# Kernel tuning notes

Measured on AMD Instinct MI355X. Metric: run time of the kernel, lower is better.

The kernel has to match this reference:

```python
import jax, jax.numpy as jnp
import numpy as np

N0 = 16384; F_IN = 384; H = 512; E0 = 131072
DEPTH = 2; RATIO = 0.25; START_K = 6; K_INC = 1; INTERP_K = 6


def _pdist2(a, b):
    # squared euclidean distances [Na, Nb]
    d2 = jnp.sum(a * a, axis=1)[:, None] + jnp.sum(b * b, axis=1)[None, :] - 2.0 * (a @ b.T)
    return jnp.maximum(d2, 0.0)


def _fps(pos, n_keep):
    # farthest point sampling, deterministic start at node 0
    sel0 = jnp.zeros((n_keep,), jnp.int32)
    dist0 = jnp.sum((pos - pos[0]) ** 2, axis=-1)

    def body(i, st):
        sel, dist = st
        idx = jnp.argmax(dist).astype(jnp.int32)
        sel = sel.at[i].set(idx)
        dist = jnp.minimum(dist, jnp.sum((pos - pos[idx]) ** 2, axis=-1))
        return (sel, dist)

    sel, _ = jax.lax.fori_loop(1, n_keep, body, (sel0, dist0))
    return sel


def _knn_graph(pos, k):
    n = pos.shape[0]
    d2 = _pdist2(pos, pos)
    d2 = d2.at[jnp.arange(n), jnp.arange(n)].set(1e10)  # exclude self
    _, nbr = jax.lax.top_k(-d2, k)                      # [n, k] nearest neighbors
    src = nbr.reshape(-1)                               # flow: source_to_target
    dst = jnp.repeat(jnp.arange(n, dtype=nbr.dtype), k)
    return src, dst


def _gcn(x, src, dst, W, b):
    # GCNConv(improved=True): A_hat = D^-1/2 (A + 2I) D^-1/2, edge weights = 1
    n = x.shape[0]
    h = x @ W
    deg = jax.ops.segment_sum(jnp.ones(src.shape[0], x.dtype), dst, num_segments=n) + 2.0
    dinv = jax.lax.rsqrt(deg)
    coef = dinv[src] * dinv[dst]
    agg = jax.ops.segment_sum(h[src] * coef[:, None], dst, num_segments=n)
    agg = agg + h * (2.0 * dinv * dinv)[:, None]        # self loops with weight 2
    return agg + b


def _knn_interpolate(x, pos_x, pos_y, k):
    # interpolate coarse features x at pos_x onto fine positions pos_y (PyG knn_interpolate)
    d2 = _pdist2(pos_y, pos_x)                          # [Ny, Nx]
    negd, idx = jax.lax.top_k(-d2, k)                   # k nearest coarse points
    w = 1.0 / jnp.maximum(-negd, 1e-16)                 # [Ny, k]
    num = jnp.einsum('yk,ykf->yf', w, x[idx])
    return num / jnp.sum(w, axis=-1, keepdims=True)


def setup_inputs() -> dict:
    key = jax.random.key(0)
    ks = jax.random.split(key, 16)
    def w(k, fin, fout):
        return (jax.random.normal(k, (fin, fout), jnp.float32) / np.sqrt(fin)).astype(jnp.float32)
    return {
        'x': jax.random.normal(ks[0], (N0, F_IN), jnp.float32),
        'pos': jax.random.uniform(ks[1], (N0, 2), jnp.float32) * 100.0,
        'edge_index': jax.random.randint(ks[2], (2, E0), 0, N0, dtype=jnp.int32),
        'W_down0': w(ks[3], F_IN, H), 'b_down0': jnp.zeros((H,), jnp.float32),
        'W_down1': w(ks[4], H, H),   'b_down1': jnp.zeros((H,), jnp.float32),
        'W_up0': w(ks[5], H, H),     'b_up0': jnp.zeros((H,), jnp.float32),
        'W_up1': w(ks[6], H, H),     'b_up1': jnp.zeros((H,), jnp.float32),
        'W_lin': w(ks[7], H, H),     'b_lin': jnp.zeros((H,), jnp.float32),
    }


def reference(x, pos, edge_index, W_down0, b_down0, W_down1, b_down1,
              W_up0, b_up0, W_up1, b_up1, W_lin, b_lin):
    src, dst = edge_index[0], edge_index[1]
    Wd = [(W_down0, b_down0), (W_down1, b_down1)]
    Wu = [(W_up0, b_up0), (W_up1, b_up1)]
    all_pos = [pos]
    all_edges = [(src, dst)]
    for i in range(DEPTH):
        x = jax.nn.relu(_gcn(x, src, dst, *Wd[i]))
        n_keep = int(x.shape[0] * RATIO)
        perm = _fps(jax.lax.stop_gradient(pos), n_keep)
        pos = pos[perm]
        src, dst = _knn_graph(pos, START_K + i * K_INC)
        x = x[perm]
        all_pos.append(pos)
        all_edges.append((src, dst))
    for i in range(DEPTH):
        x = _knn_interpolate(x, all_pos[-i - 1], all_pos[-i - 2], INTERP_K)
        s, d = all_edges[-i - 2]
        x = jax.nn.relu(_gcn(x, s, d, *Wu[i]))
    return x @ W_lin + b_lin
```

## Files before the change

### kernel.cpp

```cpp
#include <hip/hip_runtime.h>

#define N0 16384
#define N1 4096
#define N2 1024
#define E0C 131072
#define FIN 384
#define HF 512

__device__ inline float4 f4fma(float w, const float4 v, float4 a) {
  a.x = fmaf(w, v.x, a.x); a.y = fmaf(w, v.y, a.y);
  a.z = fmaf(w, v.z, a.z); a.w = fmaf(w, v.w, a.w);
  return a;
}

__global__ __launch_bounds__(256)
void count_deg(const int* __restrict__ dst, int* __restrict__ cnt, int E) {
  int e = blockIdx.x * 256 + threadIdx.x;
  if (e < E) atomicAdd(&cnt[dst[e]], 1);
}

__global__ __launch_bounds__(1024)
void scan_offsets(const int* __restrict__ cnt, int* __restrict__ offs,
                  float* __restrict__ dinv) {
  __shared__ int ts[1024];
  const int t = threadIdx.x;
  int local[16];
  int sum = 0;
  #pragma unroll
  for (int j = 0; j < 16; ++j) { local[j] = cnt[t * 16 + j]; sum += local[j]; }
  ts[t] = sum;
  __syncthreads();
  for (int off = 1; off < 1024; off <<= 1) {
    int v = (t >= off) ? ts[t - off] : 0;
    __syncthreads();
    ts[t] += v;
    __syncthreads();
  }
  int run = ts[t] - sum;
  #pragma unroll
  for (int j = 0; j < 16; ++j) {
    offs[t * 16 + j] = run;
    dinv[t * 16 + j] = 1.0f / sqrtf((float)local[j] + 2.0f);
    run += local[j];
  }
  if (t == 1023) offs[N0] = run;
}

__global__ __launch_bounds__(256)
void fill_csr(const int* __restrict__ src, const int* __restrict__ dst,
              const int* __restrict__ offs, int* __restrict__ cursor,
              int* __restrict__ srcl, int E) {
  int e = blockIdx.x * 256 + threadIdx.x;
  if (e < E) {
    int d = dst[e];
    int p = atomicAdd(&cursor[d], 1);
    srcl[offs[d] + p] = src[e];
  }
}

template<int BM, int BN, int BK>
__global__ __launch_bounds__(256)
void gemm_f32(const float* __restrict__ A, const float* __restrict__ W,
              const float* __restrict__ bias, float* __restrict__ C,
              int M, int N, int K, int addBias) {
  __shared__ float As[BK][BM + 4];
  __shared__ float Ws[BK][BN];
  const int tid = threadIdx.x;
  const int bm = blockIdx.x * BM;
  const int bn = blockIdx.y * BN;
  const int tx = tid & 15;
  const int ty = tid >> 4;
  float acc[8][4];
  #pragma unroll
  for (int i = 0; i < 8; ++i)
    #pragma unroll
    for (int j = 0; j < 4; ++j) acc[i][j] = 0.f;

  for (int k0 = 0; k0 < K; k0 += BK) {
    #pragma unroll
    for (int h = 0; h < (BM * BK) / (256 * 4); ++h) {
      int q = tid + h * 256;
      int r = q >> 2;
      int c = (q & 3) << 2;
      float4 v = *(const float4*)(A + (size_t)(bm + r) * K + k0 + c);
      As[c][r] = v.x; As[c + 1][r] = v.y; As[c + 2][r] = v.z; As[c + 3][r] = v.w;
    }
    {
      int kk = tid >> 4;
      int n = (tid & 15) << 2;
      *(float4*)(&Ws[kk][n]) = *(const float4*)(W + (size_t)(k0 + kk) * N + bn + n);
    }
    __syncthreads();
    #pragma unroll
    for (int kk = 0; kk < BK; ++kk) {
      float4 b4 = *(const float4*)(&Ws[kk][tx << 2]);
      float4 a0 = *(const float4*)(&As[kk][ty << 3]);
      float4 a1 = *(const float4*)(&As[kk][(ty << 3) + 4]);
      float a[8] = {a0.x, a0.y, a0.z, a0.w, a1.x, a1.y, a1.z, a1.w};
      float b[4] = {b4.x, b4.y, b4.z, b4.w};
      #pragma unroll
      for (int i = 0; i < 8; ++i)
        #pragma unroll
        for (int j = 0; j < 4; ++j)
          acc[i][j] = fmaf(a[i], b[j], acc[i][j]);
    }
    __syncthreads();
  }
  #pragma unroll
  for (int i = 0; i < 8; ++i) {
    int row = bm + (ty << 3) + i;
    float4 o = {acc[i][0], acc[i][1], acc[i][2], acc[i][3]};
    if (addBias) {
      const float4 bb = *(const float4*)(bias + bn + (tx << 2));
      o.x += bb.x; o.y += bb.y; o.z += bb.z; o.w += bb.w;
    }
    *(float4*)(C + (size_t)row * N + bn + (tx << 2)) = o;
  }
}

__global__ __launch_bounds__(256)
void gcn_agg_csr(const float* __restrict__ h, const int* __restrict__ offs,
                 const int* __restrict__ srcl, const float* __restrict__ dinv,
                 const float* __restrict__ bias, float* __restrict__ out, int n) {
  const int wid = threadIdx.x >> 6, lane = threadIdx.x & 63;
  const int node = blockIdx.x * 4 + wid;
  if (node >= n) return;
  const float di = dinv[node];
  const int s0 = offs[node], s1 = offs[node + 1];
  float4 a0 = {0, 0, 0, 0}, a1 = {0, 0, 0, 0};
  for (int e = s0; e < s1; ++e) {
    const int s = srcl[e];
    const float w = dinv[s] * di;
    const float4* r = (const float4*)(h + (size_t)s * HF);
    a0 = f4fma(w, r[lane], a0);
    a1 = f4fma(w, r[64 + lane], a1);
  }
  const float sw = 2.0f * di * di;
  const float4* rs = (const float4*)(h + (size_t)node * HF);
  a0 = f4fma(sw, rs[lane], a0);
  a1 = f4fma(sw, rs[64 + lane], a1);
  const float4 b0 = *(const float4*)(bias + (lane << 2));
  const float4 b1 = *(const float4*)(bias + 256 + (lane << 2));
  a0.x = fmaxf(a0.x + b0.x, 0.f); a0.y = fmaxf(a0.y + b0.y, 0.f);
  a0.z = fmaxf(a0.z + b0.z, 0.f); a0.w = fmaxf(a0.w + b0.w, 0.f);
  a1.x = fmaxf(a1.x + b1.x, 0.f); a1.y = fmaxf(a1.y + b1.y, 0.f);
  a1.z = fmaxf(a1.z + b1.z, 0.f); a1.w = fmaxf(a1.w + b1.w, 0.f);
  float4* o = (float4*)(out + (size_t)node * HF);
  o[lane] = a0; o[64 + lane] = a1;
}

template<int K>
__global__ __launch_bounds__(256)
void gcn_agg_knn(const float* __restrict__ h, const int* __restrict__ nbr,
                 const float* __restrict__ bias, float* __restrict__ out, int n) {
  const int wid = threadIdx.x >> 6, lane = threadIdx.x & 63;
  const int node = blockIdx.x * 4 + wid;
  if (node >= n) return;
  const float di = 1.0f / sqrtf((float)(K + 2));
  const float w = di * di;
  float4 a0 = {0, 0, 0, 0}, a1 = {0, 0, 0, 0};
  #pragma unroll
  for (int j = 0; j < K; ++j) {
    const int s = nbr[node * K + j];
    const float4* r = (const float4*)(h + (size_t)s * HF);
    a0 = f4fma(w, r[lane], a0);
    a1 = f4fma(w, r[64 + lane], a1);
  }
  const float sw = 2.0f * di * di;
  const float4* rs = (const float4*)(h + (size_t)node * HF);
  a0 = f4fma(sw, rs[lane], a0);
  a1 = f4fma(sw, rs[64 + lane], a1);
  const float4 b0 = *(const float4*)(bias + (lane << 2));
  const float4 b1 = *(const float4*)(bias + 256 + (lane << 2));
  a0.x = fmaxf(a0.x + b0.x, 0.f); a0.y = fmaxf(a0.y + b0.y, 0.f);
  a0.z = fmaxf(a0.z + b0.z, 0.f); a0.w = fmaxf(a0.w + b0.w, 0.f);
  a1.x = fmaxf(a1.x + b1.x, 0.f); a1.y = fmaxf(a1.y + b1.y, 0.f);
  a1.z = fmaxf(a1.z + b1.z, 0.f); a1.w = fmaxf(a1.w + b1.w, 0.f);
  float4* o = (float4*)(out + (size_t)node * HF);
  o[lane] = a0; o[64 + lane] = a1;
}

__global__ __launch_bounds__(256)
void bin_hist(const float* __restrict__ pos, int* __restrict__ cid,
              int* __restrict__ hist, int n) {
  int i = blockIdx.x * 256 + threadIdx.x;
  if (i >= n) return;
  float x = pos[2 * i], y = pos[2 * i + 1];
  int cxi = (int)(x * 0.32f); cxi = cxi < 0 ? 0 : (cxi > 31 ? 31 : cxi);
  int cyi = (int)(y * 0.32f); cyi = cyi < 0 ? 0 : (cyi > 31 ? 31 : cyi);
  int c = cyi * 32 + cxi;
  cid[i] = c;
  atomicAdd(&hist[c], 1);
}

__global__ __launch_bounds__(1024)
void bin_scan(const int* __restrict__ hist, int* __restrict__ offs) {
  __shared__ int ts[1024];
  const int t = threadIdx.x;
  int v = hist[t];
  ts[t] = v;
  __syncthreads();
  for (int off = 1; off < 1024; off <<= 1) {
    int u = (t >= off) ? ts[t - off] : 0;
    __syncthreads();
    ts[t] += u;
    __syncthreads();
  }
  offs[t] = ts[t] - v;
  if (t == 1023) offs[1024] = ts[t];
}

__global__ __launch_bounds__(256)
void bin_scatter(const float* __restrict__ pos, const int* __restrict__ cid,
                 const int* __restrict__ offs, int* __restrict__ cursor,
                 float* __restrict__ sx, float* __restrict__ sy,
                 int* __restrict__ sid, int n) {
  int i = blockIdx.x * 256 + threadIdx.x;
  if (i >= n) return;
  int c = cid[i];
  int p = atomicAdd(&cursor[c], 1);
  int slot = offs[c] + p;
  sx[slot] = pos[2 * i];
  sy[slot] = pos[2 * i + 1];
  sid[slot] = i;
}

template<int NN>
__device__ __forceinline__ unsigned ror16(unsigned v) {
  return (unsigned)__builtin_amdgcn_update_dpp(0, (int)v, 0x120 | NN, 0xF, 0xF, false);
}

__device__ __forceinline__ void kcmp(unsigned& hi, unsigned& lo, float& x, float& y,
                                     unsigned ohi, unsigned olo, float ox, float oy) {
  unsigned long long a = ((unsigned long long)hi << 32) | lo;
  unsigned long long b = ((unsigned long long)ohi << 32) | olo;
  if (b > a) { hi = ohi; lo = olo; x = ox; y = oy; }
}

#define ROR_STEP(NN) { \
    unsigned ohi_ = ror16<NN>(hi), olo_ = ror16<NN>(lo); \
    unsigned ox_ = ror16<NN>(__float_as_uint(x)), oy_ = ror16<NN>(__float_as_uint(y)); \
    kcmp(hi, lo, x, y, ohi_, olo_, __uint_as_float(ox_), __uint_as_float(oy_)); }

template<bool WENT>
__device__ __forceinline__ void entry_reduce(unsigned long long ckey, float ccx, float ccy,
                                             int t, float4* wsc,
                                             unsigned& ehi, unsigned& elo,
                                             float& ex, float& ey) {
  unsigned hi = (unsigned)(ckey >> 32), lo = (unsigned)ckey;
  float x = ccx, y = ccy;
  ROR_STEP(1) ROR_STEP(2) ROR_STEP(4) ROR_STEP(8)
  if constexpr (WENT) {
    if ((t & 15) == 0)
      wsc[(t >> 4) & 3] = make_float4(__uint_as_float(hi), __uint_as_float(lo), x, y);
    float4 a0 = wsc[0], a1 = wsc[1], a2 = wsc[2], a3 = wsc[3];
    hi = __float_as_uint(a0.x); lo = __float_as_uint(a0.y); x = a0.z; y = a0.w;
    kcmp(hi, lo, x, y, __float_as_uint(a1.x), __float_as_uint(a1.y), a1.z, a1.w);
    kcmp(hi, lo, x, y, __float_as_uint(a2.x), __float_as_uint(a2.y), a2.z, a2.w);
    kcmp(hi, lo, x, y, __float_as_uint(a3.x), __float_as_uint(a3.y), a3.z, a3.w);
  }
  ehi = hi; elo = lo; ex = x; ey = y;
}

template<int N, int NT, int NKEEP>
__global__ __launch_bounds__(NT)
void fps_fast2(const float* __restrict__ pos0,
               const float* __restrict__ sx, const float* __restrict__ sy,
               const int* __restrict__ sid,
               int* __restrict__ perm, float* __restrict__ pos_out) {
  constexpr int CHUNK = N / NT;
  constexpr int NWAVE = NT / 64;
  constexpr bool WENT = (NWAVE == 16);
  const int t = threadIdx.x;
  const int base = t * CHUNK;

  __shared__ float pxl[N];
  __shared__ float pyl[N];
  __shared__ float4 ebuf[2][16];
  __shared__ float4 wscr[NWAVE][4];

  unsigned long long key[CHUNK];
  float cx = pos0[0], cy = pos0[1];
  if (t == 0) { perm[0] = 0; pos_out[0] = cx; pos_out[1] = cy; }

  float bx0 = 3.4e38f, bx1 = -3.4e38f, by0 = 3.4e38f, by1 = -3.4e38f;
  unsigned long long ckey = 0; float ccx = 0.f, ccy = 0.f;
  #pragma unroll
  for (int j = 0; j < CHUNK; ++j) {
    float qx = sx[base + j], qy = sy[base + j];
    unsigned uid = ~(unsigned)sid[base + j];
    pxl[j * NT + t] = qx; pyl[j * NT + t] = qy;
    bx0 = fminf(bx0, qx); bx1 = fmaxf(bx1, qx);
    by0 = fminf(by0, qy); by1 = fmaxf(by1, qy);
    float dx = __fsub_rn(qx, cx), dy = __fsub_rn(qy, cy);
    float nd = __fadd_rn(__fmul_rn(dx, dx), __fmul_rn(dy, dy));
    unsigned long long k = ((unsigned long long)__float_as_uint(nd) << 32) | uid;
    key[j] = k;
    if (k > ckey) { ckey = k; ccx = qx; ccy = qy; }
  }
  float cmax = __uint_as_float((unsigned)(ckey >> 32));

  unsigned ehi, elo; float ex, ey;
  entry_reduce<WENT>(ckey, ccx, ccy, t, wscr[t >> 6], ehi, elo, ex, ey);
  if ((t & (WENT ? 63 : 15)) == 0)
    ebuf[0][WENT ? (t >> 6) : (t >> 4)] =
        make_float4(__uint_as_float(ehi), __uint_as_float(elo), ex, ey);
  __syncthreads();

  int p = 0;
  for (int i = 1; i < NKEEP; ++i) {
    float4 e = ebuf[p][t & 15];
    unsigned hi = __float_as_uint(e.x), lo = __float_as_uint(e.y);
    float x = e.z, y = e.w;
    ROR_STEP(1) ROR_STEP(2) ROR_STEP(4) ROR_STEP(8)
    if (t == 0) {
      perm[i] = (int)(~lo);
      pos_out[2 * i] = x; pos_out[2 * i + 1] = y;
    }
    cx = x; cy = y;

    float mdx = fmaxf(fmaxf(__fsub_rn(bx0, cx), __fsub_rn(cx, bx1)), 0.f);
    float mdy = fmaxf(fmaxf(__fsub_rn(by0, cy), __fsub_rn(cy, by1)), 0.f);
    float mb = mdx * mdx + mdy * mdy;
    bool act = !(mb * 0.99999f > cmax);
    if (__ballot(act) != 0) {
      if (act) {
        unsigned long long best = 0; float bx = 0.f, by = 0.f;
        #pragma unroll
        for (int j = 0; j < CHUNK; ++j) {
          float qx = pxl[j * NT + t], qy = pyl[j * NT + t];
          float dx = __fsub_rn(qx, cx), dy = __fsub_rn(qy, cy);
          float nd = __fadd_rn(__fmul_rn(dx, dx), __fmul_rn(dy, dy));
          unsigned long long nk =
              ((unsigned long long)__float_as_uint(nd) << 32) | (unsigned)key[j];
          if (nk < key[j]) key[j] = nk;
          if (key[j] > best) { best = key[j]; bx = qx; by = qy; }
        }
        ckey = best; ccx = bx; ccy = by;
        cmax = __uint_as_float((unsigned)(best >> 32));
      }
      entry_reduce<WENT>(ckey, ccx, ccy, t, wscr[t >> 6], ehi, elo, ex, ey);
    }
    if ((t & (WENT ? 63 : 15)) == 0)
      ebuf[p ^ 1][WENT ? (t >> 6) : (t >> 4)] =
          make_float4(__uint_as_float(ehi), __uint_as_float(elo), ex, ey);
    __syncthreads();
    p ^= 1;
  }
}

__global__ __launch_bounds__(256)
void gather_rows(const float* __restrict__ xin, const int* __restrict__ perm,
                 float* __restrict__ xout, int n) {
  const int wid = threadIdx.x >> 6, lane = threadIdx.x & 63;
  const int i = blockIdx.x * 4 + wid;
  if (i >= n) return;
  const int s = perm[i];
  const float4* r = (const float4*)(xin + (size_t)s * HF);
  float4* o = (float4*)(xout + (size_t)i * HF);
  o[lane] = r[lane];
  o[64 + lane] = r[64 + lane];
}

template<int NPTS, int K>
__global__ __launch_bounds__(256)
void knn_graph_kernel(const float* __restrict__ pos, int* __restrict__ srcout) {
  __shared__ float sx[NPTS], sy[NPTS], ss[NPTS];
  const int tid = threadIdx.x;
  for (int idx = tid; idx < NPTS; idx += 256) {
    float x = pos[2 * idx], y = pos[2 * idx + 1];
    sx[idx] = x; sy[idx] = y;
    ss[idx] = __fadd_rn(__fmul_rn(x, x), __fmul_rn(y, y));
  }
  __syncthreads();
  const int q = blockIdx.x * 256 + tid;
  const float qx = sx[q], qy = sy[q], qs = ss[q];
  float bd[K]; int bi[K];
  #pragma unroll
  for (int m = 0; m < K; ++m) { bd[m] = 3.4e38f; bi[m] = 0; }
  for (int j = 0; j < NPTS; ++j) {
    if (j == q) continue;
    float dot = __fadd_rn(__fmul_rn(qx, sx[j]), __fmul_rn(qy, sy[j]));
    float d2 = fmaxf(__fsub_rn(__fadd_rn(qs, ss[j]), __fmul_rn(2.0f, dot)), 0.0f);
    if (d2 < bd[K - 1]) {
      bool pr[K];
      #pragma unroll
      for (int m = 0; m < K; ++m) pr[m] = (d2 < bd[m]);
      #pragma unroll
      for (int m = K - 1; m >= 1; --m) {
        bd[m] = pr[m] ? (pr[m - 1] ? bd[m - 1] : d2) : bd[m];
        bi[m] = pr[m] ? (pr[m - 1] ? bi[m - 1] : j) : bi[m];
      }
      if (pr[0]) { bd[0] = d2; bi[0] = j; }
    }
  }
  #pragma unroll
  for (int m = 0; m < K; ++m) srcout[q * K + m] = bi[m];
}

template<int NX, int K>
__global__ __launch_bounds__(256)
void interp_topk(const float* __restrict__ posy, const float* __restrict__ posx,
                 int* __restrict__ oidx, float* __restrict__ ow,
                 float* __restrict__ owsum) {
  __shared__ float sx[NX], sy[NX], ss[NX];
  const int tid = threadIdx.x;
  for (int idx = tid; idx < NX; idx += 256) {
    float x = posx[2 * idx], y = posx[2 * idx + 1];
    sx[idx] = x; sy[idx] = y;
    ss[idx] = __fadd_rn(__fmul_rn(x, x), __fmul_rn(y, y));
  }
  __syncthreads();
  const int q = blockIdx.x * 256 + tid;
  const float qx = posy[2 * q], qy = posy[2 * q + 1];
  const float qs = __fadd_rn(__fmul_rn(qx, qx), __fmul_rn(qy, qy));
  float bd[K]; int bi[K];
  #pragma unroll
  for (int m = 0; m < K; ++m) { bd[m] = 3.4e38f; bi[m] = 0; }
  for (int j = 0; j < NX; ++j) {
    float dot = __fadd_rn(__fmul_rn(qx, sx[j]), __fmul_rn(qy, sy[j]));
    float d2 = fmaxf(__fsub_rn(__fadd_rn(qs, ss[j]), __fmul_rn(2.0f, dot)), 0.0f);
    if (d2 < bd[K - 1]) {
      bool pr[K];
      #pragma unroll
      for (int m = 0; m < K; ++m) pr[m] = (d2 < bd[m]);
      #pragma unroll
      for (int m = K - 1; m >= 1; --m) {
        bd[m] = pr[m] ? (pr[m - 1] ? bd[m - 1] : d2) : bd[m];
        bi[m] = pr[m] ? (pr[m - 1] ? bi[m - 1] : j) : bi[m];
      }
      if (pr[0]) { bd[0] = d2; bi[0] = j; }
    }
  }
  float wsum = 0.f;
  #pragma unroll
  for (int m = 0; m < K; ++m) {
    float w = 1.0f / fmaxf(bd[m], 1e-16f);
    ow[q * K + m] = w;
    oidx[q * K + m] = bi[m];
    wsum = __fadd_rn(wsum, w);
  }
  owsum[q] = wsum;
}

template<int K>
__global__ __launch_bounds__(256)
void interp_combine(const float* __restrict__ xin, const int* __restrict__ idx,
                    const float* __restrict__ w, const float* __restrict__ wsum,
                    float* __restrict__ out, int ny) {
  const int wid = threadIdx.x >> 6, lane = threadIdx.x & 63;
  const int q = blockIdx.x * 4 + wid;
  if (q >= ny) return;
  float4 a0 = {0, 0, 0, 0}, a1 = {0, 0, 0, 0};
  #pragma unroll
  for (int m = 0; m < K; ++m) {
    const int s = idx[q * K + m];
    const float wk = w[q * K + m];
    const float4* r = (const float4*)(xin + (size_t)s * HF);
    a0 = f4fma(wk, r[lane], a0);
    a1 = f4fma(wk, r[64 + lane], a1);
  }
  const float inv = wsum[q];
  a0.x /= inv; a0.y /= inv; a0.z /= inv; a0.w /= inv;
  a1.x /= inv; a1.y /= inv; a1.z /= inv; a1.w /= inv;
  float4* o = (float4*)(out + (size_t)q * HF);
  o[lane] = a0; o[64 + lane] = a1;
}

extern "C" void kernel_launch(void* const* d_in, const int* in_sizes, int n_in,
                              void* d_out, int out_size, void* d_ws, size_t ws_size,
                              hipStream_t stream) {
  const float* x    = (const float*)d_in[0];
  const float* pos  = (const float*)d_in[1];
  const int*   ei   = (const int*)d_in[2];
  const float* Wd0  = (const float*)d_in[3];
  const float* bd0  = (const float*)d_in[4];
  const float* Wd1  = (const float*)d_in[5];
  const float* bd1  = (const float*)d_in[6];
  const float* Wu0  = (const float*)d_in[7];
  const float* bu0  = (const float*)d_in[8];
  const float* Wu1  = (const float*)d_in[9];
  const float* bu1  = (const float*)d_in[10];
  const float* Wl   = (const float*)d_in[11];
  const float* bl   = (const float*)d_in[12];
  float* out = (float*)d_out;

  char* ws = (char*)d_ws;
  size_t off = 0;
  auto alloc = [&](size_t bytes) -> char* {
    char* p = ws + off;
    off = (off + bytes + 255) & ~(size_t)255;
    return p;
  };
  float* bufA   = (float*)alloc((size_t)N0 * HF * 4);
  float* bufB   = (float*)alloc((size_t)N0 * HF * 4);
  float* bufC   = (float*)alloc((size_t)N1 * HF * 4);
  float* x2     = (float*)alloc((size_t)N2 * HF * 4);
  int*   offs0  = (int*)alloc((N0 + 1) * 4);
  int*   srcl0  = (int*)alloc(E0C * 4);
  int*   cnt    = (int*)alloc(N0 * 4);
  int*   cursor = (int*)alloc(N0 * 4);
  float* dinv0  = (float*)alloc(N0 * 4);
  int*   perm0  = (int*)alloc(N1 * 4);
  float* pos1   = (float*)alloc(N1 * 2 * 4);
  int*   src1   = (int*)alloc(N1 * 6 * 4);
  int*   perm1  = (int*)alloc(N2 * 4);
  float* pos2   = (float*)alloc(N2 * 2 * 4);
  int*   iidx   = (int*)alloc((size_t)N0 * 6 * 4);
  float* iw     = (float*)alloc((size_t)N0 * 6 * 4);
  float* iwsum  = (float*)alloc(N0 * 4);
  float* bsx    = (float*)alloc(N0 * 4);
  float* bsy    = (float*)alloc(N0 * 4);
  int*   bsid   = (int*)alloc(N0 * 4);
  int*   bcid   = (int*)alloc(N0 * 4);
  int*   bhist  = (int*)alloc(1024 * 4);
  int*   bcur   = (int*)alloc(1024 * 4);
  int*   boffs  = (int*)alloc(1025 * 4);

  float* h1   = bufB;
  float* x1f  = bufB + (size_t)N1 * HF;
  float* hu0  = bufB;
  float* xu0f = bufB + (size_t)N1 * HF;

  hipMemsetAsync(cnt, 0, N0 * 4, stream);
  hipMemsetAsync(cursor, 0, N0 * 4, stream);
  count_deg<<<E0C / 256, 256, 0, stream>>>(ei + E0C, cnt, E0C);
  scan_offsets<<<1, 1024, 0, stream>>>(cnt, offs0, dinv0);
  fill_csr<<<E0C / 256, 256, 0, stream>>>(ei, ei + E0C, offs0, cursor, srcl0, E0C);

  hipMemsetAsync(bhist, 0, 1024 * 4, stream);
  hipMemsetAsync(bcur, 0, 1024 * 4, stream);
  bin_hist<<<N0 / 256, 256, 0, stream>>>(pos, bcid, bhist, N0);
  bin_scan<<<1, 1024, 0, stream>>>(bhist, boffs);
  bin_scatter<<<N0 / 256, 256, 0, stream>>>(pos, bcid, boffs, bcur, bsx, bsy, bsid, N0);

  gemm_f32<128, 64, 16><<<dim3(N0 / 128, HF / 64), 256, 0, stream>>>(
      x, Wd0, nullptr, bufA, N0, HF, FIN, 0);
  gcn_agg_csr<<<N0 / 4, 256, 0, stream>>>(bufA, offs0, srcl0, dinv0, bd0, bufB, N0);
  fps_fast2<N0, 1024, N1><<<1, 1024, 0, stream>>>(pos, bsx, bsy, bsid, perm0, pos1);
  gather_rows<<<N1 / 4, 256, 0, stream>>>(bufB, perm0, bufC, N1);
  knn_graph_kernel<N1, 6><<<N1 / 256, 256, 0, stream>>>(pos1, src1);

  hipMemsetAsync(bhist, 0, 1024 * 4, stream);
  hipMemsetAsync(bcur, 0, 1024 * 4, stream);
  bin_hist<<<N1 / 256, 256, 0, stream>>>(pos1, bcid, bhist, N1);
  bin_scan<<<1, 1024, 0, stream>>>(bhist, boffs);
  bin_scatter<<<N1 / 256, 256, 0, stream>>>(pos1, bcid, boffs, bcur, bsx, bsy, bsid, N1);

  gemm_f32<128, 64, 16><<<dim3(N1 / 128, HF / 64), 256, 0, stream>>>(
      bufC, Wd1, nullptr, h1, N1, HF, HF, 0);
  gcn_agg_knn<6><<<N1 / 4, 256, 0, stream>>>(h1, src1, bd1, x1f, N1);
  fps_fast2<N1, 256, N2><<<1, 256, 0, stream>>>(pos1, bsx, bsy, bsid, perm1, pos2);
  gather_rows<<<N2 / 4, 256, 0, stream>>>(x1f, perm1, x2, N2);

  interp_topk<N2, 6><<<N1 / 256, 256, 0, stream>>>(pos1, pos2, iidx, iw, iwsum);
  interp_combine<6><<<N1 / 4, 256, 0, stream>>>(x2, iidx, iw, iwsum, bufC, N1);
  gemm_f32<128, 64, 16><<<dim3(N1 / 128, HF / 64), 256, 0, stream>>>(
      bufC, Wu0, nullptr, hu0, N1, HF, HF, 0);
  gcn_agg_knn<6><<<N1 / 4, 256, 0, stream>>>(hu0, src1, bu0, xu0f, N1);

  interp_topk<N1, 6><<<N0 / 256, 256, 0, stream>>>(pos, pos1, iidx, iw, iwsum);
  interp_combine<6><<<N0 / 4, 256, 0, stream>>>(xu0f, iidx, iw, iwsum, bufA, N0);
  gemm_f32<128, 64, 16><<<dim3(N0 / 128, HF / 64), 256, 0, stream>>>(
      bufA, Wu1, nullptr, bufB, N0, HF, HF, 0);
  gcn_agg_csr<<<N0 / 4, 256, 0, stream>>>(bufB, offs0, srcl0, dinv0, bu1, bufA, N0);

  gemm_f32<128, 64, 16><<<dim3(N0 / 128, HF / 64), 256, 0, stream>>>(
      bufA, Wl, bl, out, N0, HF, HF, 1);
}
```

Measured before the change: 9.260 ms.

## Use Morton-ordered binning and wave-level bounding-box culling in FPS

Bins are now numbered in Z-order (Morton) instead of row-major, so each thread's chunk and each wave's span of points are spatially compact. The FPS kernel computes a per-wave bounding box and skips a whole wave's update when the new centre cannot reduce that wave's maximum distance. It also packs positions into float2 in shared memory and runs the second-level FPS with 512 threads instead of 256. The cost is an extra shuffle reduction at startup and an LDS cross-wave step in every wave reduction. Correctness relies on the 0.99999 safety margin still holding for the coarser wave-level bound.

Measured after the change: 8.442 ms. 1.1x faster.

```diff
diff --git a/kernel.cpp b/kernel.cpp
--- a/kernel.cpp
+++ b/kernel.cpp
@@ -180,6 +180,15 @@
   o[lane] = a0; o[64 + lane] = a1;
 }
 
+__device__ __forceinline__ unsigned part1by1(unsigned x) {
+  x &= 0xFFFFu;
+  x = (x | (x << 8)) & 0x00FF00FFu;
+  x = (x | (x << 4)) & 0x0F0F0F0Fu;
+  x = (x | (x << 2)) & 0x33333333u;
+  x = (x | (x << 1)) & 0x55555555u;
+  return x;
+}
+
 __global__ __launch_bounds__(256)
 void bin_hist(const float* __restrict__ pos, int* __restrict__ cid,
               int* __restrict__ hist, int n) {
@@ -188,7 +197,7 @@
   float x = pos[2 * i], y = pos[2 * i + 1];
   int cxi = (int)(x * 0.32f); cxi = cxi < 0 ? 0 : (cxi > 31 ? 31 : cxi);
   int cyi = (int)(y * 0.32f); cyi = cyi < 0 ? 0 : (cyi > 31 ? 31 : cyi);
-  int c = cyi * 32 + cxi;
+  int c = (int)(part1by1((unsigned)cxi) | (part1by1((unsigned)cyi) << 1));
   cid[i] = c;
   atomicAdd(&hist[c], 1);
 }
@@ -242,42 +251,38 @@
     unsigned ox_ = ror16<NN>(__float_as_uint(x)), oy_ = ror16<NN>(__float_as_uint(y)); \
     kcmp(hi, lo, x, y, ohi_, olo_, __uint_as_float(ox_), __uint_as_float(oy_)); }
 
-template<bool WENT>
-__device__ __forceinline__ void entry_reduce(unsigned long long ckey, float ccx, float ccy,
-                                             int t, float4* wsc,
-                                             unsigned& ehi, unsigned& elo,
-                                             float& ex, float& ey) {
+__device__ __forceinline__ void wave_entry_reduce(
+    unsigned long long ckey, float ccx, float ccy, int t, float4* wsc,
+    unsigned& ehi, unsigned& elo, float& ex, float& ey) {
   unsigned hi = (unsigned)(ckey >> 32), lo = (unsigned)ckey;
   float x = ccx, y = ccy;
   ROR_STEP(1) ROR_STEP(2) ROR_STEP(4) ROR_STEP(8)
-  if constexpr (WENT) {
-    if ((t & 15) == 0)
-      wsc[(t >> 4) & 3] = make_float4(__uint_as_float(hi), __uint_as_float(lo), x, y);
-    float4 a0 = wsc[0], a1 = wsc[1], a2 = wsc[2], a3 = wsc[3];
-    hi = __float_as_uint(a0.x); lo = __float_as_uint(a0.y); x = a0.z; y = a0.w;
-    kcmp(hi, lo, x, y, __float_as_uint(a1.x), __float_as_uint(a1.y), a1.z, a1.w);
-    kcmp(hi, lo, x, y, __float_as_uint(a2.x), __float_as_uint(a2.y), a2.z, a2.w);
-    kcmp(hi, lo, x, y, __float_as_uint(a3.x), __float_as_uint(a3.y), a3.z, a3.w);
-  }
+  if ((t & 15) == 0)
+    wsc[(t >> 4) & 3] = make_float4(__uint_as_float(hi), __uint_as_float(lo), x, y);
+  float4 a0 = wsc[0], a1 = wsc[1], a2 = wsc[2], a3 = wsc[3];
+  hi = __float_as_uint(a0.x); lo = __float_as_uint(a0.y); x = a0.z; y = a0.w;
+  kcmp(hi, lo, x, y, __float_as_uint(a1.x), __float_as_uint(a1.y), a1.z, a1.w);
+  kcmp(hi, lo, x, y, __float_as_uint(a2.x), __float_as_uint(a2.y), a2.z, a2.w);
+  kcmp(hi, lo, x, y, __float_as_uint(a3.x), __float_as_uint(a3.y), a3.z, a3.w);
   ehi = hi; elo = lo; ex = x; ey = y;
 }
 
 template<int N, int NT, int NKEEP>
 __global__ __launch_bounds__(NT)
-void fps_fast2(const float* __restrict__ pos0,
+void fps_fast3(const float* __restrict__ pos0,
                const float* __restrict__ sx, const float* __restrict__ sy,
                const int* __restrict__ sid,
                int* __restrict__ perm, float* __restrict__ pos_out) {
   constexpr int CHUNK = N / NT;
-  constexpr int NWAVE = NT / 64;
-  constexpr bool WENT = (NWAVE == 16);
+  constexpr int NW = NT / 64;
   const int t = threadIdx.x;
+  const int wid = t >> 6;
+  const int lane = t & 63;
   const int base = t * CHUNK;
 
-  __shared__ float pxl[N];
-  __shared__ float pyl[N];
-  __shared__ float4 ebuf[2][16];
-  __shared__ float4 wscr[NWAVE][4];
+  __shared__ float2 pp[N];
+  __shared__ float4 ebuf[2][NW];
+  __shared__ float4 wscr[NW][4];
 
   unsigned long long key[CHUNK];
   float cx = pos0[0], cy = pos0[1];
@@ -289,7 +294,7 @@
   for (int j = 0; j < CHUNK; ++j) {
     float qx = sx[base + j], qy = sy[base + j];
     unsigned uid = ~(unsigned)sid[base + j];
-    pxl[j * NT + t] = qx; pyl[j * NT + t] = qy;
+    pp[j * NT + t] = make_float2(qx, qy);
     bx0 = fminf(bx0, qx); bx1 = fmaxf(bx1, qx);
     by0 = fminf(by0, qy); by1 = fmaxf(by1, qy);
     float dx = __fsub_rn(qx, cx), dy = __fsub_rn(qy, cy);
@@ -300,50 +305,65 @@
   }
   float cmax = __uint_as_float((unsigned)(ckey >> 32));
 
+  float wx0 = bx0, wx1 = bx1, wy0 = by0, wy1 = by1;
+  #pragma unroll
+  for (int m = 1; m < 64; m <<= 1) {
+    wx0 = fminf(wx0, __shfl_xor(wx0, m));
+    wx1 = fmaxf(wx1, __shfl_xor(wx1, m));
+    wy0 = fminf(wy0, __shfl_xor(wy0, m));
+    wy1 = fmaxf(wy1, __shfl_xor(wy1, m));
+  }
+
   unsigned ehi, elo; float ex, ey;
-  entry_reduce<WENT>(ckey, ccx, ccy, t, wscr[t >> 6], ehi, elo, ex, ey);
-  if ((t & (WENT ? 63 : 15)) == 0)
-    ebuf[0][WENT ? (t >> 6) : (t >> 4)] =
-        make_float4(__uint_as_float(ehi), __uint_as_float(elo), ex, ey);
+  wave_entry_reduce(ckey, ccx, ccy, t, wscr[wid], ehi, elo, ex, ey);
+  if (lane == 0)
+    ebuf[0][wid] = make_float4(__uint_as_float(ehi), __uint_as_float(elo), ex, ey);
   __syncthreads();
 
   int p = 0;
   for (int i = 1; i < NKEEP; ++i) {
-    float4 e = ebuf[p][t & 15];
+    float4 e = ebuf[p][t & (NW - 1)];
     unsigned hi = __float_as_uint(e.x), lo = __float_as_uint(e.y);
     float x = e.z, y = e.w;
-    ROR_STEP(1) ROR_STEP(2) ROR_STEP(4) ROR_STEP(8)
+    ROR_STEP(1) ROR_STEP(2)
+    if constexpr (NW >= 8) { ROR_STEP(4) }
+    if constexpr (NW >= 16) { ROR_STEP(8) }
     if (t == 0) {
       perm[i] = (int)(~lo);
       pos_out[2 * i] = x; pos_out[2 * i + 1] = y;
     }
     cx = x; cy = y;
 
-    float mdx = fmaxf(fmaxf(__fsub_rn(bx0, cx), __fsub_rn(cx, bx1)), 0.f);
-    float mdy = fmaxf(fmaxf(__fsub_rn(by0, cy), __fsub_rn(cy, by1)), 0.f);
-    float mb = mdx * mdx + mdy * mdy;
-    bool act = !(mb * 0.99999f > cmax);
-    if (__ballot(act) != 0) {
-      if (act) {
-        unsigned long long best = 0; float bx = 0.f, by = 0.f;
-        #pragma unroll
-        for (int j = 0; j < CHUNK; ++j) {
-          float qx = pxl[j * NT + t], qy = pyl[j * NT + t];
-          float dx = __fsub_rn(qx, cx), dy = __fsub_rn(qy, cy);
-          float nd = __fadd_rn(__fmul_rn(dx, dx), __fmul_rn(dy, dy));
-          unsigned long long nk =
-              ((unsigned long long)__float_as_uint(nd) << 32) | (unsigned)key[j];
-          if (nk < key[j]) key[j] = nk;
-          if (key[j] > best) { best = key[j]; bx = qx; by = qy; }
+    float wmdx = fmaxf(fmaxf(__fsub_rn(wx0, cx), __fsub_rn(cx, wx1)), 0.f);
+    float wmdy = fmaxf(fmaxf(__fsub_rn(wy0, cy), __fsub_rn(cy, wy1)), 0.f);
+    float wmb = wmdx * wmdx + wmdy * wmdy;
+    float wcmax = __uint_as_float(ehi);
+    if (!(wmb * 0.99999f > wcmax)) {
+      float mdx = fmaxf(fmaxf(__fsub_rn(bx0, cx), __fsub_rn(cx, bx1)), 0.f);
+      float mdy = fmaxf(fmaxf(__fsub_rn(by0, cy), __fsub_rn(cy, by1)), 0.f);
+      float mb = mdx * mdx + mdy * mdy;
+      bool act = !(mb * 0.99999f > cmax);
+      if (__ballot(act) != 0) {
+        if (act) {
+          unsigned long long best = 0; float bx = 0.f, by = 0.f;
+          #pragma unroll
+          for (int j = 0; j < CHUNK; ++j) {
+            float2 q = pp[j * NT + t];
+            float dx = __fsub_rn(q.x, cx), dy = __fsub_rn(q.y, cy);
+            float nd = __fadd_rn(__fmul_rn(dx, dx), __fmul_rn(dy, dy));
+            unsigned long long nk =
+                ((unsigned long long)__float_as_uint(nd) << 32) | (unsigned)key[j];
+            if (nk < key[j]) key[j] = nk;
+            if (key[j] > best) { best = key[j]; bx = q.x; by = q.y; }
+          }
+          ckey = best; ccx = bx; ccy = by;
+          cmax = __uint_as_float((unsigned)(best >> 32));
         }
-        ckey = best; ccx = bx; ccy = by;
-        cmax = __uint_as_float((unsigned)(best >> 32));
+        wave_entry_reduce(ckey, ccx, ccy, t, wscr[wid], ehi, elo, ex, ey);
       }
-      entry_reduce<WENT>(ckey, ccx, ccy, t, wscr[t >> 6], ehi, elo, ex, ey);
-    }
-    if ((t & (WENT ? 63 : 15)) == 0)
-      ebuf[p ^ 1][WENT ? (t >> 6) : (t >> 4)] =
-          make_float4(__uint_as_float(ehi), __uint_as_float(elo), ex, ey);
+    }
+    if (lane == 0)
+      ebuf[p ^ 1][wid] = make_float4(__uint_as_float(ehi), __uint_as_float(elo), ex, ey);
     __syncthreads();
     p ^= 1;
   }
@@ -537,7 +557,7 @@
   gemm_f32<128, 64, 16><<<dim3(N0 / 128, HF / 64), 256, 0, stream>>>(
       x, Wd0, nullptr, bufA, N0, HF, FIN, 0);
   gcn_agg_csr<<<N0 / 4, 256, 0, stream>>>(bufA, offs0, srcl0, dinv0, bd0, bufB, N0);
-  fps_fast2<N0, 1024, N1><<<1, 1024, 0, stream>>>(pos, bsx, bsy, bsid, perm0, pos1);
+  fps_fast3<N0, 1024, N1><<<1, 1024, 0, stream>>>(pos, bsx, bsy, bsid, perm0, pos1);
   gather_rows<<<N1 / 4, 256, 0, stream>>>(bufB, perm0, bufC, N1);
   knn_graph_kernel<N1, 6><<<N1 / 256, 256, 0, stream>>>(pos1, src1);
 
@@ -550,7 +570,7 @@
   gemm_f32<128, 64, 16><<<dim3(N1 / 128, HF / 64), 256, 0, stream>>>(
       bufC, Wd1, nullptr, h1, N1, HF, HF, 0);
   gcn_agg_knn<6><<<N1 / 4, 256, 0, stream>>>(h1, src1, bd1, x1f, N1);
-  fps_fast2<N1, 256, N2><<<1, 256, 0, stream>>>(pos1, bsx, bsy, bsid, perm1, pos2);
+  fps_fast3<N1, 512, N2><<<1, 512, 0, stream>>>(pos1, bsx, bsy, bsid, perm1, pos2);
   gather_rows<<<N2 / 4, 256, 0, stream>>>(x1f, perm1, x2, N2);
 
   interp_topk<N2, 6><<<N1 / 256, 256, 0, stream>>>(pos1, pos2, iidx, iw, iwsum);
```
